# Kernel optimization log

Measured on AMD Instinct MI355X. Metric: run time of the kernel, lower is better.

The kernel has to match this reference:

```python
import jax, jax.numpy as jnp
import numpy as np

B, T, I, H = 32, 1024, 1024, 1024


def _init_cell(key, in_size, hidden):
    k = 1.0 / np.sqrt(hidden)
    k1, k2, k3, k4 = jax.random.split(key, 4)
    Wih = jax.random.uniform(k1, (4 * hidden, in_size), jnp.float32, -k, k)
    Whh = jax.random.uniform(k2, (4 * hidden, hidden), jnp.float32, -k, k)
    bih = jax.random.uniform(k3, (4 * hidden,), jnp.float32, -k, k)
    bhh = jax.random.uniform(k4, (4 * hidden,), jnp.float32, -k, k)
    return Wih, Whh, bih, bhh


def setup_inputs() -> dict:
    key = jax.random.key(0)
    kx, kf, kr = jax.random.split(key, 3)
    x = jax.random.normal(kx, (B, T, I), jnp.float32)
    h0 = jnp.zeros((B, H), jnp.float32)
    c0 = jnp.zeros((B, H), jnp.float32)
    Wih_f, Whh_f, bih_f, bhh_f = _init_cell(kf, I, H)
    Wih_r, Whh_r, bih_r, bhh_r = _init_cell(kr, I, H)
    return {"x": x, "h0": h0, "c0": c0,
            "Wih_f": Wih_f, "Whh_f": Whh_f, "bih_f": bih_f, "bhh_f": bhh_f,
            "Wih_r": Wih_r, "Whh_r": Whh_r, "bih_r": bih_r, "bhh_r": bhh_r}


def _lstm_scan(xs, h0, c0, Wih, Whh, bih, bhh, reverse):
    # xs: [T, B, I]; PyTorch LSTMCell gate order: i, f, g, o
    def step(carry, xt):
        h, c = carry
        gates = xt @ Wih.T + bih + h @ Whh.T + bhh  # [B, 4H]
        i, f, g, o = jnp.split(gates, 4, axis=-1)
        c_new = jax.nn.sigmoid(f) * c + jax.nn.sigmoid(i) * jnp.tanh(g)
        h_new = jax.nn.sigmoid(o) * jnp.tanh(c_new)
        return (h_new, c_new), None

    (hT, cT), _ = jax.lax.scan(step, (h0, c0), xs, reverse=reverse)
    return hT, cT


def reference(x, h0, c0, Wih_f, Whh_f, bih_f, bhh_f, Wih_r, Whh_r, bih_r, bhh_r):
    xs = jnp.swapaxes(x, 0, 1)  # [T, B, I]
    hf, _ = _lstm_scan(xs, h0, c0, Wih_f, Whh_f, bih_f, bhh_f, reverse=False)
    # reversed(x.unbind(1)) == processing time steps from T-1 down to 0
    hr, _ = _lstm_scan(xs, h0, c0, Wih_r, Whh_r, bih_r, bhh_r, reverse=True)
    return (hf, hr)
```

## Files before the change

### kernel.cpp

```cpp
#include <hip/hip_runtime.h>
#include <hip/hip_bf16.h>
#include <cstdint>
#include <cstddef>

typedef unsigned short u16;
typedef unsigned long long u64;
typedef __attribute__((ext_vector_type(8))) short short8;
typedef __attribute__((ext_vector_type(4))) float f32x4;
typedef __attribute__((ext_vector_type(4))) unsigned u32x4;

#define NB 32
#define NT 1024
#define NH 1024
#define TCH 128
#define NCH 8

#define O_XB   0ull
#define O_WIH  67108864ull
#define O_WHHP 83886080ull
#define O_BIAS 117440512ull
#define O_HBUF 117473280ull
#define O_CST  117735424ull
#define O_FLG  117997568ull
#define O_GX   118030336ull
#define DSTRIDE_CH   16777216ull
#define DSTRIDE_HALF 33554432ull
#define DSTRIDE_FULL 134217728ull
#define WS_NEED_HALF (O_GX + 2ull * DSTRIDE_HALF * 2ull)
#define WS_NEED_FULL (O_GX + 2ull * DSTRIDE_FULL * 2ull)

__device__ __forceinline__ u16 f2bf(float f){
  union { float f; unsigned u; } v; v.f = f;
  unsigned r = v.u + 0x7FFFu + ((v.u >> 16) & 1u);
  return (u16)(r >> 16);
}
__device__ __forceinline__ float bf2f(u16 h){
  union { unsigned u; float f; } v; v.u = ((unsigned)h) << 16;
  return v.f;
}
__device__ __forceinline__ float sig_f(float x){ return 1.0f / (1.0f + __expf(-x)); }
__device__ __forceinline__ float tanh_f(float x){ return 1.0f - 2.0f / (1.0f + __expf(2.0f * x)); }

__device__ __forceinline__ void g2l16(const void* g, void* l){
  __builtin_amdgcn_global_load_lds(
      (const __attribute__((address_space(1))) unsigned int*)g,
      (__attribute__((address_space(3))) unsigned int*)l, 16, 0, 0);
}
__device__ __forceinline__ void g2l16c(const void* g, void* l){
  __builtin_amdgcn_global_load_lds(
      (const __attribute__((address_space(1))) unsigned int*)g,
      (__attribute__((address_space(3))) unsigned int*)l, 16, 0, 17);
}
__device__ __forceinline__ void store16_llc(void* p, u32x4 v){
  asm volatile("global_store_dwordx4 %0, %1, off sc0 sc1"
               :: "v"((unsigned long long)(uintptr_t)p), "v"(v) : "memory");
}

__device__ __forceinline__ float sel4(float s0, float s1, float s2, float s3, int k){
  float a = (k & 1) ? s1 : s0;
  float b = (k & 1) ? s3 : s2;
  return (k & 2) ? b : a;
}

__device__ __forceinline__ int img_off(int lr, int bo){
  return lr * 2048 + (bo ^ ((((lr & 7) ^ ((bo >> 8) & 7))) << 4));
}

__global__ void k_cvt(const float* __restrict__ src, u16* __restrict__ dst, int n){
  int i = (blockIdx.x * blockDim.x + threadIdx.x) * 4;
  int stride = gridDim.x * blockDim.x * 4;
  for (; i < n; i += stride){
    float4 v = *(const float4*)(src + i);
    uint2 p;
    p.x = (unsigned)f2bf(v.x) | ((unsigned)f2bf(v.y) << 16);
    p.y = (unsigned)f2bf(v.z) | ((unsigned)f2bf(v.w) << 16);
    *(uint2*)(dst + i) = p;
  }
}

__global__ void k_pack_whh(const float* __restrict__ whh_f, const float* __restrict__ whh_r,
                           u16* __restrict__ dst){
  int bx = blockIdx.x;
  int dir = bx >> 8, rem = bx & 255;
  int jg = rem >> 1, ni = rem & 1;
  const float* whh = dir ? whh_r : whh_f;
  int tid = threadIdx.x;
  int lane = tid & 63, wq = tid >> 6;
  int c = lane & 15;
  int n = (c >> 2) * 1024 + jg * 8 + ni * 4 + (c & 3);
  int kkb = (lane >> 4) * 8;
  size_t fb = ((((size_t)dir * 128 + jg) * 2 + ni) * 32) * 2;
  for (int q = 0; q < 8; q++){
    int ks = wq * 8 + q;
    const float4* p = (const float4*)(whh + (size_t)n * 1024 + ks * 32 + kkb);
    float4 w0 = p[0], w1 = p[1];
    float w[8] = {w0.x, w0.y, w0.z, w0.w, w1.x, w1.y, w1.z, w1.w};
    unsigned hh[4], ll[4];
    #pragma unroll
    for (int e = 0; e < 4; e++){
      u16 h0 = f2bf(w[2*e]),   l0 = f2bf(w[2*e]   - bf2f(f2bf(w[2*e])));
      u16 h1 = f2bf(w[2*e+1]), l1 = f2bf(w[2*e+1] - bf2f(f2bf(w[2*e+1])));
      hh[e] = (unsigned)h0 | ((unsigned)h1 << 16);
      ll[e] = (unsigned)l0 | ((unsigned)l1 << 16);
    }
    uint4* dh = (uint4*)(dst + (fb + (size_t)ks * 2 + 0) * 512 + lane * 8);
    uint4* dl = (uint4*)(dst + (fb + (size_t)ks * 2 + 1) * 512 + lane * 8);
    *dh = make_uint4(hh[0], hh[1], hh[2], hh[3]);
    *dl = make_uint4(ll[0], ll[1], ll[2], ll[3]);
  }
}

__global__ void k_init(const float* __restrict__ h0, const float* __restrict__ c0,
                       const float* __restrict__ bih_f, const float* __restrict__ bhh_f,
                       const float* __restrict__ bih_r, const float* __restrict__ bhh_r,
                       char* __restrict__ hbuf, float* __restrict__ cst,
                       float* __restrict__ bias, int* __restrict__ flg){
  int i = blockIdx.x * blockDim.x + threadIdx.x;
  int stride = gridDim.x * blockDim.x;
  for (int k = i; k < 32768; k += stride){
    int b = k >> 10, j = k & 1023;
    int lr = b & 15, mhb = b >> 4;
    u16 v = f2bf(h0[k]);
    int off = img_off(lr, 2 * j);
    *(u16*)(hbuf + (size_t)((0 * 2 + mhb) * 2) * 32768 + off) = v;
    *(u16*)(hbuf + (size_t)((1 * 2 + mhb) * 2) * 32768 + off) = v;
    float cv = c0[k];
    cst[k] = cv;
    cst[32768 + k] = cv;
  }
  for (int k = i; k < 8192; k += stride){
    if (k < 4096) bias[k] = bih_f[k] + bhh_f[k];
    else          bias[k] = bih_r[k - 4096] + bhh_r[k - 4096];
  }
  for (int k = i; k < 8192; k += stride) flg[k] = 0;
}

__global__ __launch_bounds__(256, 2) void k_gemm(const u16* __restrict__ xb,
                                                 const u16* __restrict__ wih,
                                                 const float* __restrict__ bias,
                                                 u16* __restrict__ gx, int chunk,
                                                 int tOff, size_t dirStride){
  __shared__ u16 smem[2 * 16384];
  const int tid = threadIdx.x;
  const int lane = tid & 63, wid = tid >> 6;
  const int mi = wid >> 1, ni = wid & 1;
  const int c = lane & 15, rg = lane >> 4;
  const int n0 = blockIdx.x * 128;
  const int m0 = blockIdx.y * 128;
  const int dir = blockIdx.z;
  const u16* wd = wih + (size_t)dir * 4194304;

  f32x4 acc[4][4] = {};

  auto stage = [&](int buf, int k0){
    #pragma unroll
    for (int q = 0; q < 8; q++){
      int f = wid * 8 + q;
      int ks = f & 1;
      int kk = k0 + ks * 32 + rg * 8;
      const u16* src;
      if (f < 16){
        int rowloc = (f >> 1) * 16 + c;
        int tl = (m0 + rowloc) >> 5;
        int bb = rowloc & 31;
        int tg = dir ? (1023 - chunk * TCH - tl) : (chunk * TCH + tl);
        src = xb + (size_t)(bb * 1024 + tg) * 1024 + kk;
      } else {
        int nt = (f - 16) >> 1;
        src = wd + (size_t)(n0 + nt * 16 + c) * 1024 + kk;
      }
      g2l16((const void*)src, (void*)(smem + buf * 16384 + f * 512));
    }
  };

  stage(0, 0);
  asm volatile("s_waitcnt vmcnt(0)" ::: "memory");
  __syncthreads();

  for (int it = 0; it < 16; it++){
    int cur = it & 1;
    if (it < 15) stage(cur ^ 1, (it + 1) * 64);
    const u16* bp = smem + cur * 16384;
    #pragma unroll
    for (int ks = 0; ks < 2; ks++){
      short8 a[4], b[4];
      #pragma unroll
      for (int im = 0; im < 4; im++)
        a[im] = *(const short8*)(bp + ((mi * 4 + im) * 2 + ks) * 512 + lane * 8);
      #pragma unroll
      for (int in_ = 0; in_ < 4; in_++)
        b[in_] = *(const short8*)(bp + 8192 + ((ni * 4 + in_) * 2 + ks) * 512 + lane * 8);
      #pragma unroll
      for (int im = 0; im < 4; im++)
        #pragma unroll
        for (int in_ = 0; in_ < 4; in_++)
          acc[im][in_] = __builtin_amdgcn_mfma_f32_16x16x32_bf16(a[im], b[in_], acc[im][in_], 0, 0, 0);
    }
    asm volatile("s_waitcnt vmcnt(0)" ::: "memory");
    __syncthreads();
  }

  u16* T = (u16*)smem;
  const float* bd = bias + dir * 4096;
  #pragma unroll
  for (int in_ = 0; in_ < 4; in_++){
    int nnLocal = (ni * 4 + in_) * 16 + c;
    float bv = bd[n0 + nnLocal];
    #pragma unroll
    for (int im = 0; im < 4; im++){
      #pragma unroll
      for (int r = 0; r < 4; r++){
        int row = (mi * 4 + im) * 16 + rg * 4 + r;
        T[row * 128 + nnLocal] = f2bf(acc[im][in_][r] + bv);
      }
    }
  }
  __syncthreads();
  u16* gxd = gx + (size_t)dir * dirStride;
  const int nprBase = ((n0 & 1023) >> 3) * 32 + ((n0 >> 10) << 3);
  #pragma unroll
  for (int q = 0; q < 8; q++){
    int flat = q * 256 + tid;
    int row = flat >> 4, c16 = flat & 15;
    u32x4 v = *(const u32x4*)(T + row * 128 + c16 * 8);
    *(u32x4*)(gxd + (size_t)(tOff * 32 + m0 + row) * 4096 + nprBase + c16 * 32) = v;
  }
}

__global__ __launch_bounds__(256, 1) void k_rnn(const u16* __restrict__ gx,
                                                const u16* __restrict__ whhp,
                                                char* __restrict__ hbuf,
                                                float* __restrict__ cstate,
                                                float* __restrict__ dout,
                                                int* __restrict__ flg,
                                                int s0, int bar0, int nsteps,
                                                size_t dirStride){
  __shared__ char smem[32768];
  __shared__ __align__(16) u16 tb[16][16];
  __shared__ int lflag[2];
  const int tid = threadIdx.x;
  const int lane = tid & 63, wid = tid >> 6;
  const int bx = blockIdx.x;
  const int dir = bx >> 7, mh = (bx >> 6) & 1, ug = bx & 63;
  const int grp = dir * 2 + mh;
  const int c = lane & 15, rg = lane >> 4;
  const int g = c >> 2, jj = c & 3;
  const int u = ug * 16 + wid * 4 + jj;
  const int jg = ug * 2 + (wid >> 1), ni = wid & 1;

  short8 Bhi[32], Blo[32];
  {
    size_t fb = ((((size_t)dir * 128 + jg) * 2 + ni) * 32) * 2;
    #pragma unroll
    for (int ks = 0; ks < 32; ks++){
      Bhi[ks] = *(const short8*)(whhp + (fb + ks * 2 + 0) * 512 + lane * 8);
      Blo[ks] = *(const short8*)(whhp + (fb + ks * 2 + 1) * 512 + lane * 8);
    }
  }

  float cst[4];
  #pragma unroll
  for (int r = 0; r < 4; r++)
    cst[r] = cstate[(size_t)dir * 32768 + (size_t)(mh * 16 + rg * 4 + r) * 1024 + u];

  const int npr = (u >> 3) * 32 + g * 8 + (u & 7);
  int* flags = flg + grp * 2048;

  if (tid == 0){ lflag[0] = 0; lflag[1] = 0; }
  __syncthreads();

  u16 gxu[4];
  {
    const size_t gof = (size_t)dir * dirStride + npr;
    #pragma unroll
    for (int r = 0; r < 4; r++)
      gxu[r] = gx[gof + (size_t)(mh * 16 + rg * 4 + r) * 4096];
  }

  for (int t = 0; t < nsteps; t++){
    const int s = s0 + t;
    const char* img_r = hbuf + (size_t)(grp * 2 + (s & 1)) * 32768;
    char* img_w = hbuf + (size_t)(grp * 2 + ((s + 1) & 1)) * 32768;
    const unsigned tgt = (unsigned)(bar0 + t);

    if (wid == 0){
      if (t > 0){
        int* fp = flags + (lane & 31) * 32;
        while (true){
          int v = __hip_atomic_load(fp, __ATOMIC_RELAXED, __HIP_MEMORY_SCOPE_AGENT);
          if (__all((unsigned)v >= tgt)) break;
        }
        asm volatile("" ::: "memory");
      }
      #pragma unroll
      for (int i = 0; i < 16; i++)
        g2l16c(img_r + i * 2048 + lane * 16, smem + i * 2048 + lane * 16);
      asm volatile("s_waitcnt vmcnt(0)" ::: "memory");
      __hip_atomic_store(&lflag[0], t + 1, __ATOMIC_RELEASE, __HIP_MEMORY_SCOPE_WORKGROUP);
    } else if (wid == 1){
      if (t > 0){
        int* fp = flags + (32 + (lane & 31)) * 32;
        while (true){
          int v = __hip_atomic_load(fp, __ATOMIC_RELAXED, __HIP_MEMORY_SCOPE_AGENT);
          if (__all((unsigned)v >= tgt)) break;
        }
        asm volatile("" ::: "memory");
      }
      #pragma unroll
      for (int i = 0; i < 16; i++)
        g2l16c(img_r + i * 2048 + 1024 + lane * 16, smem + i * 2048 + 1024 + lane * 16);
      asm volatile("s_waitcnt vmcnt(0)" ::: "memory");
      __hip_atomic_store(&lflag[1], t + 1, __ATOMIC_RELEASE, __HIP_MEMORY_SCOPE_WORKGROUP);
    }

    u16 gxn[4];
    if (t < nsteps - 1){
      const size_t gof = (size_t)dir * dirStride + (size_t)(t + 1) * 131072 + npr;
      #pragma unroll
      for (int r = 0; r < 4; r++)
        gxn[r] = gx[gof + (size_t)(mh * 16 + rg * 4 + r) * 4096];
    }

    f32x4 ah = {0.f,0.f,0.f,0.f}, al = {0.f,0.f,0.f,0.f};
    const int abase = c * 2048;
    while (__hip_atomic_load(&lflag[0], __ATOMIC_ACQUIRE, __HIP_MEMORY_SCOPE_WORKGROUP) < t + 1) {}
    __builtin_amdgcn_sched_barrier(0);
    #pragma unroll
    for (int ks = 0; ks < 16; ks++){
      int b = ks * 64 + rg * 16;
      int addr = abase + (b ^ ((((c & 7) ^ ((b >> 8) & 7))) << 4));
      short8 a = *(const short8*)(smem + addr);
      ah = __builtin_amdgcn_mfma_f32_16x16x32_bf16(a, Bhi[ks], ah, 0, 0, 0);
      al = __builtin_amdgcn_mfma_f32_16x16x32_bf16(a, Blo[ks], al, 0, 0, 0);
    }
    while (__hip_atomic_load(&lflag[1], __ATOMIC_ACQUIRE, __HIP_MEMORY_SCOPE_WORKGROUP) < t + 1) {}
    __builtin_amdgcn_sched_barrier(0);
    #pragma unroll
    for (int ks = 16; ks < 32; ks++){
      int b = ks * 64 + rg * 16;
      int addr = abase + (b ^ ((((c & 7) ^ ((b >> 8) & 7))) << 4));
      short8 a = *(const short8*)(smem + addr);
      ah = __builtin_amdgcn_mfma_f32_16x16x32_bf16(a, Bhi[ks], ah, 0, 0, 0);
      al = __builtin_amdgcn_mfma_f32_16x16x32_bf16(a, Blo[ks], al, 0, 0, 0);
    }

    #pragma unroll
    for (int r = 0; r < 4; r++){
      float v = (ah[r] + al[r]) + bf2f(gxu[r]);
      float act = (g == 2) ? tanh_f(v) : sig_f(v);
      float a4  = __int_as_float(__builtin_amdgcn_ds_swizzle(__float_as_int(act), 0x101F));
      float a8  = __int_as_float(__builtin_amdgcn_ds_swizzle(__float_as_int(act), 0x201F));
      float a12 = __int_as_float(__builtin_amdgcn_ds_swizzle(__float_as_int(act), 0x301F));
      float i_s = sel4(act, a4, a8, a12, g);
      float f_s = sel4(act, a4, a8, a12, g ^ 1);
      float g_t = sel4(act, a4, a8, a12, g ^ 2);
      float o_s = sel4(act, a4, a8, a12, g ^ 3);
      float cn = f_s * cst[r] + i_s * g_t;
      cst[r] = cn;
      float hn = o_s * tanh_f(cn);
      if (g == 0){
        int lr = rg * 4 + r;
        tb[lr][wid * 4 + jj] = f2bf(hn);
        if (s == 1023)
          dout[(size_t)dir * 32768 + (size_t)(mh * 16 + lr) * 1024 + u] = hn;
        if (t == nsteps - 1)
          cstate[(size_t)dir * 32768 + (size_t)(mh * 16 + lr) * 1024 + u] = cn;
      }
    }
    __syncthreads();

    if (wid == 3){
      if (lane < 32){
        int lr = lane >> 1, half = lane & 1;
        u32x4 v = *(const u32x4*)&tb[lr][half * 8];
        store16_llc(img_w + img_off(lr, ug * 32 + half * 16), v);
      }
      asm volatile("s_waitcnt vmcnt(0)" ::: "memory");
      if (lane == 0 && t < nsteps - 1)
        __hip_atomic_store(&flags[ug * 32], bar0 + t + 1,
                           __ATOMIC_RELAXED, __HIP_MEMORY_SCOPE_AGENT);
    }

    if (t < nsteps - 1){
      #pragma unroll
      for (int r = 0; r < 4; r++) gxu[r] = gxn[r];
    }
  }
}

extern "C" void kernel_launch(void* const* d_in, const int* in_sizes, int n_in,
                              void* d_out, int out_size, void* d_ws, size_t ws_size,
                              hipStream_t stream){
  const float* x     = (const float*)d_in[0];
  const float* h0    = (const float*)d_in[1];
  const float* c0    = (const float*)d_in[2];
  const float* Wih_f = (const float*)d_in[3];
  const float* Whh_f = (const float*)d_in[4];
  const float* bih_f = (const float*)d_in[5];
  const float* bhh_f = (const float*)d_in[6];
  const float* Wih_r = (const float*)d_in[7];
  const float* Whh_r = (const float*)d_in[8];
  const float* bih_r = (const float*)d_in[9];
  const float* bhh_r = (const float*)d_in[10];
  float* out = (float*)d_out;

  char* ws = (char*)d_ws;
  u16*   xb    = (u16*)(ws + O_XB);
  u16*   wih   = (u16*)(ws + O_WIH);
  u16*   whhp  = (u16*)(ws + O_WHHP);
  float* bias  = (float*)(ws + O_BIAS);
  char*  hbuf  = (char*)(ws + O_HBUF);
  float* cstw  = (float*)(ws + O_CST);
  int*   flg   = (int*)(ws + O_FLG);
  u16*   gx    = (u16*)(ws + O_GX);

  k_cvt<<<2048, 256, 0, stream>>>(x, xb, 32 * 1024 * 1024);
  k_cvt<<<512, 256, 0, stream>>>(Wih_f, wih, 4096 * 1024);
  k_cvt<<<512, 256, 0, stream>>>(Wih_r, wih + 4194304, 4096 * 1024);
  k_pack_whh<<<512, 256, 0, stream>>>(Whh_f, Whh_r, whhp);
  k_init<<<64, 256, 0, stream>>>(h0, c0, bih_f, bhh_f, bih_r, bhh_r, hbuf, cstw, bias, flg);

  if (ws_size >= WS_NEED_FULL){
    for (int g = 0; g < NCH; g++)
      k_gemm<<<dim3(32, 32, 2), 256, 0, stream>>>(xb, wih, bias, gx, g,
                                                  g * TCH, (size_t)DSTRIDE_FULL);
    k_rnn<<<dim3(256), dim3(256), 0, stream>>>(gx, whhp, hbuf, cstw, out, flg,
                                               0, 0, NT, (size_t)DSTRIDE_FULL);
  } else if (ws_size >= WS_NEED_HALF){
    for (int c2 = 0; c2 < 4; c2++){
      k_gemm<<<dim3(32, 32, 2), 256, 0, stream>>>(xb, wih, bias, gx, 2 * c2,
                                                  0, (size_t)DSTRIDE_HALF);
      k_gemm<<<dim3(32, 32, 2), 256, 0, stream>>>(xb, wih, bias, gx, 2 * c2 + 1,
                                                  128, (size_t)DSTRIDE_HALF);
      k_rnn<<<dim3(256), dim3(256), 0, stream>>>(gx, whhp, hbuf, cstw, out, flg,
                                                 c2 * 256, c2 * 255, 256,
                                                 (size_t)DSTRIDE_HALF);
    }
  } else {
    for (int ch = 0; ch < NCH; ch++){
      k_gemm<<<dim3(32, 32, 2), 256, 0, stream>>>(xb, wih, bias, gx, ch,
                                                  0, (size_t)DSTRIDE_CH);
      k_rnn<<<dim3(256), dim3(256), 0, stream>>>(gx, whhp, hbuf, cstw, out, flg,
                                                 ch * TCH, ch * (TCH - 1), TCH,
                                                 (size_t)DSTRIDE_CH);
    }
  }
}
```

Baseline: 5.558 ms.

## Switch LSTM to single fp16 weights and halve recurrent grid to 128 blocks

```diff
diff --git a/kernel.cpp b/kernel.cpp
--- a/kernel.cpp
+++ b/kernel.cpp
@@ -5,7 +5,7 @@
 
 typedef unsigned short u16;
 typedef unsigned long long u64;
-typedef __attribute__((ext_vector_type(8))) short short8;
+typedef __attribute__((ext_vector_type(8))) _Float16 h8;
 typedef __attribute__((ext_vector_type(4))) float f32x4;
 typedef __attribute__((ext_vector_type(4))) unsigned u32x4;
 
@@ -29,14 +29,11 @@
 #define WS_NEED_HALF (O_GX + 2ull * DSTRIDE_HALF * 2ull)
 #define WS_NEED_FULL (O_GX + 2ull * DSTRIDE_FULL * 2ull)
 
-__device__ __forceinline__ u16 f2bf(float f){
-  union { float f; unsigned u; } v; v.f = f;
-  unsigned r = v.u + 0x7FFFu + ((v.u >> 16) & 1u);
-  return (u16)(r >> 16);
-}
-__device__ __forceinline__ float bf2f(u16 h){
-  union { unsigned u; float f; } v; v.u = ((unsigned)h) << 16;
-  return v.f;
+__device__ __forceinline__ u16 f2h(float f){
+  union { _Float16 h; u16 u; } v; v.h = (_Float16)f; return v.u;
+}
+__device__ __forceinline__ float h2f(u16 b){
+  union { u16 u; _Float16 h; } v; v.u = b; return (float)v.h;
 }
 __device__ __forceinline__ float sig_f(float x){ return 1.0f / (1.0f + __expf(-x)); }
 __device__ __forceinline__ float tanh_f(float x){ return 1.0f - 2.0f / (1.0f + __expf(2.0f * x)); }
@@ -72,8 +69,8 @@
   for (; i < n; i += stride){
     float4 v = *(const float4*)(src + i);
     uint2 p;
-    p.x = (unsigned)f2bf(v.x) | ((unsigned)f2bf(v.y) << 16);
-    p.y = (unsigned)f2bf(v.z) | ((unsigned)f2bf(v.w) << 16);
+    p.x = (unsigned)f2h(v.x) | ((unsigned)f2h(v.y) << 16);
+    p.y = (unsigned)f2h(v.z) | ((unsigned)f2h(v.w) << 16);
     *(uint2*)(dst + i) = p;
   }
 }
@@ -89,24 +86,18 @@
   int c = lane & 15;
   int n = (c >> 2) * 1024 + jg * 8 + ni * 4 + (c & 3);
   int kkb = (lane >> 4) * 8;
-  size_t fb = ((((size_t)dir * 128 + jg) * 2 + ni) * 32) * 2;
+  size_t fb = (((size_t)dir * 128 + jg) * 2 + ni) * 32;
   for (int q = 0; q < 8; q++){
     int ks = wq * 8 + q;
     const float4* p = (const float4*)(whh + (size_t)n * 1024 + ks * 32 + kkb);
     float4 w0 = p[0], w1 = p[1];
     float w[8] = {w0.x, w0.y, w0.z, w0.w, w1.x, w1.y, w1.z, w1.w};
-    unsigned hh[4], ll[4];
-    #pragma unroll
-    for (int e = 0; e < 4; e++){
-      u16 h0 = f2bf(w[2*e]),   l0 = f2bf(w[2*e]   - bf2f(f2bf(w[2*e])));
-      u16 h1 = f2bf(w[2*e+1]), l1 = f2bf(w[2*e+1] - bf2f(f2bf(w[2*e+1])));
-      hh[e] = (unsigned)h0 | ((unsigned)h1 << 16);
-      ll[e] = (unsigned)l0 | ((unsigned)l1 << 16);
-    }
-    uint4* dh = (uint4*)(dst + (fb + (size_t)ks * 2 + 0) * 512 + lane * 8);
-    uint4* dl = (uint4*)(dst + (fb + (size_t)ks * 2 + 1) * 512 + lane * 8);
+    unsigned hh[4];
+    #pragma unroll
+    for (int e = 0; e < 4; e++)
+      hh[e] = (unsigned)f2h(w[2*e]) | ((unsigned)f2h(w[2*e+1]) << 16);
+    uint4* dh = (uint4*)(dst + (fb + (size_t)ks) * 512 + lane * 8);
     *dh = make_uint4(hh[0], hh[1], hh[2], hh[3]);
-    *dl = make_uint4(ll[0], ll[1], ll[2], ll[3]);
   }
 }
 
@@ -120,7 +111,7 @@
   for (int k = i; k < 32768; k += stride){
     int b = k >> 10, j = k & 1023;
     int lr = b & 15, mhb = b >> 4;
-    u16 v = f2bf(h0[k]);
+    u16 v = f2h(h0[k]);
     int off = img_off(lr, 2 * j);
     *(u16*)(hbuf + (size_t)((0 * 2 + mhb) * 2) * 32768 + off) = v;
     *(u16*)(hbuf + (size_t)((1 * 2 + mhb) * 2) * 32768 + off) = v;
@@ -132,7 +123,7 @@
     if (k < 4096) bias[k] = bih_f[k] + bhh_f[k];
     else          bias[k] = bih_r[k - 4096] + bhh_r[k - 4096];
   }
-  for (int k = i; k < 8192; k += stride) flg[k] = 0;
+  for (int k = i; k < 4096; k += stride) flg[k] = 0;
 }
 
 __global__ __launch_bounds__(256, 2) void k_gemm(const u16* __restrict__ xb,
@@ -183,18 +174,18 @@
     const u16* bp = smem + cur * 16384;
     #pragma unroll
     for (int ks = 0; ks < 2; ks++){
-      short8 a[4], b[4];
+      h8 a[4], b[4];
       #pragma unroll
       for (int im = 0; im < 4; im++)
-        a[im] = *(const short8*)(bp + ((mi * 4 + im) * 2 + ks) * 512 + lane * 8);
+        a[im] = *(const h8*)(bp + ((mi * 4 + im) * 2 + ks) * 512 + lane * 8);
       #pragma unroll
       for (int in_ = 0; in_ < 4; in_++)
-        b[in_] = *(const short8*)(bp + 8192 + ((ni * 4 + in_) * 2 + ks) * 512 + lane * 8);
+        b[in_] = *(const h8*)(bp + 8192 + ((ni * 4 + in_) * 2 + ks) * 512 + lane * 8);
       #pragma unroll
       for (int im = 0; im < 4; im++)
         #pragma unroll
         for (int in_ = 0; in_ < 4; in_++)
-          acc[im][in_] = __builtin_amdgcn_mfma_f32_16x16x32_bf16(a[im], b[in_], acc[im][in_], 0, 0, 0);
+          acc[im][in_] = __builtin_amdgcn_mfma_f32_16x16x32_f16(a[im], b[in_], acc[im][in_], 0, 0, 0);
     }
     asm volatile("s_waitcnt vmcnt(0)" ::: "memory");
     __syncthreads();
@@ -211,7 +202,7 @@
       #pragma unroll
       for (int r = 0; r < 4; r++){
         int row = (mi * 4 + im) * 16 + rg * 4 + r;
-        T[row * 128 + nnLocal] = f2bf(acc[im][in_][r] + bv);
+        T[row * 128 + nnLocal] = f2h(acc[im][in_][r] + bv);
       }
     }
   }
@@ -236,45 +227,50 @@
                                                 int s0, int bar0, int nsteps,
                                                 size_t dirStride){
   __shared__ char smem[32768];
-  __shared__ __align__(16) u16 tb[16][16];
+  __shared__ __align__(16) u16 tb[16][32];
   __shared__ int lflag[2];
   const int tid = threadIdx.x;
   const int lane = tid & 63, wid = tid >> 6;
   const int bx = blockIdx.x;
-  const int dir = bx >> 7, mh = (bx >> 6) & 1, ug = bx & 63;
+  const int dir = bx >> 6, mh = (bx >> 5) & 1, ug = bx & 31;
   const int grp = dir * 2 + mh;
   const int c = lane & 15, rg = lane >> 4;
   const int g = c >> 2, jj = c & 3;
-  const int u = ug * 16 + wid * 4 + jj;
-  const int jg = ug * 2 + (wid >> 1), ni = wid & 1;
-
-  short8 Bhi[32], Blo[32];
+  const int jg2 = ug * 4 + wid;
+
+  h8 Bh[32][2];
   {
-    size_t fb = ((((size_t)dir * 128 + jg) * 2 + ni) * 32) * 2;
+    size_t fb0 = (((size_t)dir * 128 + jg2) * 2 + 0) * 32;
+    size_t fb1 = (((size_t)dir * 128 + jg2) * 2 + 1) * 32;
     #pragma unroll
     for (int ks = 0; ks < 32; ks++){
-      Bhi[ks] = *(const short8*)(whhp + (fb + ks * 2 + 0) * 512 + lane * 8);
-      Blo[ks] = *(const short8*)(whhp + (fb + ks * 2 + 1) * 512 + lane * 8);
-    }
-  }
-
-  float cst[4];
+      Bh[ks][0] = *(const h8*)(whhp + (fb0 + ks) * 512 + lane * 8);
+      Bh[ks][1] = *(const h8*)(whhp + (fb1 + ks) * 512 + lane * 8);
+    }
+  }
+
+  float cst[2][4];
   #pragma unroll
-  for (int r = 0; r < 4; r++)
-    cst[r] = cstate[(size_t)dir * 32768 + (size_t)(mh * 16 + rg * 4 + r) * 1024 + u];
-
-  const int npr = (u >> 3) * 32 + g * 8 + (u & 7);
-  int* flags = flg + grp * 2048;
+  for (int it = 0; it < 2; it++)
+    #pragma unroll
+    for (int r = 0; r < 4; r++)
+      cst[it][r] = cstate[(size_t)dir * 32768 +
+                          (size_t)(mh * 16 + rg * 4 + r) * 1024 + jg2 * 8 + it * 4 + jj];
+
+  const int npr0 = jg2 * 32 + g * 8 + jj;
+  int* flags = flg + grp * 1024;
 
   if (tid == 0){ lflag[0] = 0; lflag[1] = 0; }
   __syncthreads();
 
-  u16 gxu[4];
+  u16 gxu[2][4];
   {
-    const size_t gof = (size_t)dir * dirStride + npr;
-    #pragma unroll
-    for (int r = 0; r < 4; r++)
-      gxu[r] = gx[gof + (size_t)(mh * 16 + rg * 4 + r) * 4096];
+    const size_t gof = (size_t)dir * dirStride + npr0;
+    #pragma unroll
+    for (int it = 0; it < 2; it++)
+      #pragma unroll
+      for (int r = 0; r < 4; r++)
+        gxu[it][r] = gx[gof + it * 4 + (size_t)(mh * 16 + rg * 4 + r) * 4096];
   }
 
   for (int t = 0; t < nsteps; t++){
@@ -285,7 +281,7 @@
 
     if (wid == 0){
       if (t > 0){
-        int* fp = flags + (lane & 31) * 32;
+        int* fp = flags + (lane & 15) * 32;
         while (true){
           int v = __hip_atomic_load(fp, __ATOMIC_RELAXED, __HIP_MEMORY_SCOPE_AGENT);
           if (__all((unsigned)v >= tgt)) break;
@@ -299,7 +295,7 @@
       __hip_atomic_store(&lflag[0], t + 1, __ATOMIC_RELEASE, __HIP_MEMORY_SCOPE_WORKGROUP);
     } else if (wid == 1){
       if (t > 0){
-        int* fp = flags + (32 + (lane & 31)) * 32;
+        int* fp = flags + (16 + (lane & 15)) * 32;
         while (true){
           int v = __hip_atomic_load(fp, __ATOMIC_RELAXED, __HIP_MEMORY_SCOPE_AGENT);
           if (__all((unsigned)v >= tgt)) break;
@@ -313,15 +309,17 @@
       __hip_atomic_store(&lflag[1], t + 1, __ATOMIC_RELEASE, __HIP_MEMORY_SCOPE_WORKGROUP);
     }
 
-    u16 gxn[4];
+    u16 gxn[2][4];
     if (t < nsteps - 1){
-      const size_t gof = (size_t)dir * dirStride + (size_t)(t + 1) * 131072 + npr;
-      #pragma unroll
-      for (int r = 0; r < 4; r++)
-        gxn[r] = gx[gof + (size_t)(mh * 16 + rg * 4 + r) * 4096];
-    }
-
-    f32x4 ah = {0.f,0.f,0.f,0.f}, al = {0.f,0.f,0.f,0.f};
+      const size_t gof = (size_t)dir * dirStride + (size_t)(t + 1) * 131072 + npr0;
+      #pragma unroll
+      for (int it = 0; it < 2; it++)
+        #pragma unroll
+        for (int r = 0; r < 4; r++)
+          gxn[it][r] = gx[gof + it * 4 + (size_t)(mh * 16 + rg * 4 + r) * 4096];
+    }
+
+    f32x4 a0 = {0.f,0.f,0.f,0.f}, a1 = {0.f,0.f,0.f,0.f};
     const int abase = c * 2048;
     while (__hip_atomic_load(&lflag[0], __ATOMIC_ACQUIRE, __HIP_MEMORY_SCOPE_WORKGROUP) < t + 1) {}
     __builtin_amdgcn_sched_barrier(0);
@@ -329,9 +327,9 @@
     for (int ks = 0; ks < 16; ks++){
       int b = ks * 64 + rg * 16;
       int addr = abase + (b ^ ((((c & 7) ^ ((b >> 8) & 7))) << 4));
-      short8 a = *(const short8*)(smem + addr);
-      ah = __builtin_amdgcn_mfma_f32_16x16x32_bf16(a, Bhi[ks], ah, 0, 0, 0);
-      al = __builtin_amdgcn_mfma_f32_16x16x32_bf16(a, Blo[ks], al, 0, 0, 0);
+      h8 a = *(const h8*)(smem + addr);
+      a0 = __builtin_amdgcn_mfma_f32_16x16x32_f16(a, Bh[ks][0], a0, 0, 0, 0);
+      a1 = __builtin_amdgcn_mfma_f32_16x16x32_f16(a, Bh[ks][1], a1, 0, 0, 0);
     }
     while (__hip_atomic_load(&lflag[1], __ATOMIC_ACQUIRE, __HIP_MEMORY_SCOPE_WORKGROUP) < t + 1) {}
     __builtin_amdgcn_sched_barrier(0);
@@ -339,42 +337,44 @@
     for (int ks = 16; ks < 32; ks++){
       int b = ks * 64 + rg * 16;
       int addr = abase + (b ^ ((((c & 7) ^ ((b >> 8) & 7))) << 4));
-      short8 a = *(const short8*)(smem + addr);
-      ah = __builtin_amdgcn_mfma_f32_16x16x32_bf16(a, Bhi[ks], ah, 0, 0, 0);
-      al = __builtin_amdgcn_mfma_f32_16x16x32_bf16(a, Blo[ks], al, 0, 0, 0);
-    }
-
-    #pragma unroll
-    for (int r = 0; r < 4; r++){
-      float v = (ah[r] + al[r]) + bf2f(gxu[r]);
-      float act = (g == 2) ? tanh_f(v) : sig_f(v);
-      float a4  = __int_as_float(__builtin_amdgcn_ds_swizzle(__float_as_int(act), 0x101F));
-      float a8  = __int_as_float(__builtin_amdgcn_ds_swizzle(__float_as_int(act), 0x201F));
-      float a12 = __int_as_float(__builtin_amdgcn_ds_swizzle(__float_as_int(act), 0x301F));
-      float i_s = sel4(act, a4, a8, a12, g);
-      float f_s = sel4(act, a4, a8, a12, g ^ 1);
-      float g_t = sel4(act, a4, a8, a12, g ^ 2);
-      float o_s = sel4(act, a4, a8, a12, g ^ 3);
-      float cn = f_s * cst[r] + i_s * g_t;
-      cst[r] = cn;
-      float hn = o_s * tanh_f(cn);
-      if (g == 0){
-        int lr = rg * 4 + r;
-        tb[lr][wid * 4 + jj] = f2bf(hn);
-        if (s == 1023)
-          dout[(size_t)dir * 32768 + (size_t)(mh * 16 + lr) * 1024 + u] = hn;
-        if (t == nsteps - 1)
-          cstate[(size_t)dir * 32768 + (size_t)(mh * 16 + lr) * 1024 + u] = cn;
+      h8 a = *(const h8*)(smem + addr);
+      a0 = __builtin_amdgcn_mfma_f32_16x16x32_f16(a, Bh[ks][0], a0, 0, 0, 0);
+      a1 = __builtin_amdgcn_mfma_f32_16x16x32_f16(a, Bh[ks][1], a1, 0, 0, 0);
+    }
+
+    #pragma unroll
+    for (int it = 0; it < 2; it++){
+      #pragma unroll
+      for (int r = 0; r < 4; r++){
+        float v = (it ? a1[r] : a0[r]) + h2f(gxu[it][r]);
+        float act = (g == 2) ? tanh_f(v) : sig_f(v);
+        float a4  = __int_as_float(__builtin_amdgcn_ds_swizzle(__float_as_int(act), 0x101F));
+        float a8  = __int_as_float(__builtin_amdgcn_ds_swizzle(__float_as_int(act), 0x201F));
+        float a12 = __int_as_float(__builtin_amdgcn_ds_swizzle(__float_as_int(act), 0x301F));
+        float i_s = sel4(act, a4, a8, a12, g);
+        float f_s = sel4(act, a4, a8, a12, g ^ 1);
+        float g_t = sel4(act, a4, a8, a12, g ^ 2);
+        float o_s = sel4(act, a4, a8, a12, g ^ 3);
+        float cn = f_s * cst[it][r] + i_s * g_t;
+        cst[it][r] = cn;
+        float hn = o_s * tanh_f(cn);
+        if (g == 0){
+          int lr = rg * 4 + r;
+          int ub = wid * 8 + it * 4 + jj;
+          tb[lr][ub] = f2h(hn);
+          if (s == 1023)
+            dout[(size_t)dir * 32768 + (size_t)(mh * 16 + lr) * 1024 + ug * 32 + ub] = hn;
+          if (t == nsteps - 1)
+            cstate[(size_t)dir * 32768 + (size_t)(mh * 16 + lr) * 1024 + ug * 32 + ub] = cn;
+        }
       }
     }
     __syncthreads();
 
     if (wid == 3){
-      if (lane < 32){
-        int lr = lane >> 1, half = lane & 1;
-        u32x4 v = *(const u32x4*)&tb[lr][half * 8];
-        store16_llc(img_w + img_off(lr, ug * 32 + half * 16), v);
-      }
+      int lr = lane >> 2, q4 = lane & 3;
+      u32x4 v = *(const u32x4*)&tb[lr][q4 * 8];
+      store16_llc(img_w + img_off(lr, ug * 64 + q4 * 16), v);
       asm volatile("s_waitcnt vmcnt(0)" ::: "memory");
       if (lane == 0 && t < nsteps - 1)
         __hip_atomic_store(&flags[ug * 32], bar0 + t + 1,
@@ -383,7 +383,9 @@
 
     if (t < nsteps - 1){
       #pragma unroll
-      for (int r = 0; r < 4; r++) gxu[r] = gxn[r];
+      for (int it = 0; it < 2; it++)
+        #pragma unroll
+        for (int r = 0; r < 4; r++) gxu[it][r] = gxn[it][r];
     }
   }
 }
@@ -424,7 +426,7 @@
     for (int g = 0; g < NCH; g++)
       k_gemm<<<dim3(32, 32, 2), 256, 0, stream>>>(xb, wih, bias, gx, g,
                                                   g * TCH, (size_t)DSTRIDE_FULL);
-    k_rnn<<<dim3(256), dim3(256), 0, stream>>>(gx, whhp, hbuf, cstw, out, flg,
+    k_rnn<<<dim3(128), dim3(256), 0, stream>>>(gx, whhp, hbuf, cstw, out, flg,
                                                0, 0, NT, (size_t)DSTRIDE_FULL);
   } else if (ws_size >= WS_NEED_HALF){
     for (int c2 = 0; c2 < 4; c2++){
@@ -432,7 +434,7 @@
                                                   0, (size_t)DSTRIDE_HALF);
       k_gemm<<<dim3(32, 32, 2), 256, 0, stream>>>(xb, wih, bias, gx, 2 * c2 + 1,
                                                   128, (size_t)DSTRIDE_HALF);
-      k_rnn<<<dim3(256), dim3(256), 0, stream>>>(gx, whhp, hbuf, cstw, out, flg,
+      k_rnn<<<dim3(128), dim3(256), 0, stream>>>(gx, whhp, hbuf, cstw, out, flg,
                                                  c2 * 256, c2 * 255, 256,
                                                  (size_t)DSTRIDE_HALF);
     }
@@ -440,7 +442,7 @@
     for (int ch = 0; ch < NCH; ch++){
       k_gemm<<<dim3(32, 32, 2), 256, 0, stream>>>(xb, wih, bias, gx, ch,
                                                   0, (size_t)DSTRIDE_CH);
-      k_rnn<<<dim3(256), dim3(256), 0, stream>>>(gx, whhp, hbuf, cstw, out, flg,
+      k_rnn<<<dim3(128), dim3(256), 0, stream>>>(gx, whhp, hbuf, cstw, out, flg,
                                                  ch * TCH, ch * (TCH - 1), TCH,
                                                  (size_t)DSTRIDE_CH);
     }
```

Result: slower. 6.428 ms (+15.7%).

## Switch LSTM matmuls to fp16 and drop split hi/lo recurrent weights

Applied to the files above, without the earlier changes.

```diff
diff --git a/kernel.cpp b/kernel.cpp
--- a/kernel.cpp
+++ b/kernel.cpp
@@ -5,7 +5,7 @@
 
 typedef unsigned short u16;
 typedef unsigned long long u64;
-typedef __attribute__((ext_vector_type(8))) short short8;
+typedef __attribute__((ext_vector_type(8))) _Float16 h8;
 typedef __attribute__((ext_vector_type(4))) float f32x4;
 typedef __attribute__((ext_vector_type(4))) unsigned u32x4;
 
@@ -29,14 +29,11 @@
 #define WS_NEED_HALF (O_GX + 2ull * DSTRIDE_HALF * 2ull)
 #define WS_NEED_FULL (O_GX + 2ull * DSTRIDE_FULL * 2ull)
 
-__device__ __forceinline__ u16 f2bf(float f){
-  union { float f; unsigned u; } v; v.f = f;
-  unsigned r = v.u + 0x7FFFu + ((v.u >> 16) & 1u);
-  return (u16)(r >> 16);
-}
-__device__ __forceinline__ float bf2f(u16 h){
-  union { unsigned u; float f; } v; v.u = ((unsigned)h) << 16;
-  return v.f;
+__device__ __forceinline__ u16 f2h(float f){
+  union { _Float16 h; u16 u; } v; v.h = (_Float16)f; return v.u;
+}
+__device__ __forceinline__ float h2f(u16 b){
+  union { u16 u; _Float16 h; } v; v.u = b; return (float)v.h;
 }
 __device__ __forceinline__ float sig_f(float x){ return 1.0f / (1.0f + __expf(-x)); }
 __device__ __forceinline__ float tanh_f(float x){ return 1.0f - 2.0f / (1.0f + __expf(2.0f * x)); }
@@ -72,8 +69,8 @@
   for (; i < n; i += stride){
     float4 v = *(const float4*)(src + i);
     uint2 p;
-    p.x = (unsigned)f2bf(v.x) | ((unsigned)f2bf(v.y) << 16);
-    p.y = (unsigned)f2bf(v.z) | ((unsigned)f2bf(v.w) << 16);
+    p.x = (unsigned)f2h(v.x) | ((unsigned)f2h(v.y) << 16);
+    p.y = (unsigned)f2h(v.z) | ((unsigned)f2h(v.w) << 16);
     *(uint2*)(dst + i) = p;
   }
 }
@@ -89,24 +86,18 @@
   int c = lane & 15;
   int n = (c >> 2) * 1024 + jg * 8 + ni * 4 + (c & 3);
   int kkb = (lane >> 4) * 8;
-  size_t fb = ((((size_t)dir * 128 + jg) * 2 + ni) * 32) * 2;
+  size_t fb = (((size_t)dir * 128 + jg) * 2 + ni) * 32;
   for (int q = 0; q < 8; q++){
     int ks = wq * 8 + q;
     const float4* p = (const float4*)(whh + (size_t)n * 1024 + ks * 32 + kkb);
     float4 w0 = p[0], w1 = p[1];
     float w[8] = {w0.x, w0.y, w0.z, w0.w, w1.x, w1.y, w1.z, w1.w};
-    unsigned hh[4], ll[4];
-    #pragma unroll
-    for (int e = 0; e < 4; e++){
-      u16 h0 = f2bf(w[2*e]),   l0 = f2bf(w[2*e]   - bf2f(f2bf(w[2*e])));
-      u16 h1 = f2bf(w[2*e+1]), l1 = f2bf(w[2*e+1] - bf2f(f2bf(w[2*e+1])));
-      hh[e] = (unsigned)h0 | ((unsigned)h1 << 16);
-      ll[e] = (unsigned)l0 | ((unsigned)l1 << 16);
-    }
-    uint4* dh = (uint4*)(dst + (fb + (size_t)ks * 2 + 0) * 512 + lane * 8);
-    uint4* dl = (uint4*)(dst + (fb + (size_t)ks * 2 + 1) * 512 + lane * 8);
+    unsigned hh[4];
+    #pragma unroll
+    for (int e = 0; e < 4; e++)
+      hh[e] = (unsigned)f2h(w[2*e]) | ((unsigned)f2h(w[2*e+1]) << 16);
+    uint4* dh = (uint4*)(dst + (fb + (size_t)ks) * 512 + lane * 8);
     *dh = make_uint4(hh[0], hh[1], hh[2], hh[3]);
-    *dl = make_uint4(ll[0], ll[1], ll[2], ll[3]);
   }
 }
 
@@ -120,7 +111,7 @@
   for (int k = i; k < 32768; k += stride){
     int b = k >> 10, j = k & 1023;
     int lr = b & 15, mhb = b >> 4;
-    u16 v = f2bf(h0[k]);
+    u16 v = f2h(h0[k]);
     int off = img_off(lr, 2 * j);
     *(u16*)(hbuf + (size_t)((0 * 2 + mhb) * 2) * 32768 + off) = v;
     *(u16*)(hbuf + (size_t)((1 * 2 + mhb) * 2) * 32768 + off) = v;
@@ -183,18 +174,18 @@
     const u16* bp = smem + cur * 16384;
     #pragma unroll
     for (int ks = 0; ks < 2; ks++){
-      short8 a[4], b[4];
+      h8 a[4], b[4];
       #pragma unroll
       for (int im = 0; im < 4; im++)
-        a[im] = *(const short8*)(bp + ((mi * 4 + im) * 2 + ks) * 512 + lane * 8);
+        a[im] = *(const h8*)(bp + ((mi * 4 + im) * 2 + ks) * 512 + lane * 8);
       #pragma unroll
       for (int in_ = 0; in_ < 4; in_++)
-        b[in_] = *(const short8*)(bp + 8192 + ((ni * 4 + in_) * 2 + ks) * 512 + lane * 8);
+        b[in_] = *(const h8*)(bp + 8192 + ((ni * 4 + in_) * 2 + ks) * 512 + lane * 8);
       #pragma unroll
       for (int im = 0; im < 4; im++)
         #pragma unroll
         for (int in_ = 0; in_ < 4; in_++)
-          acc[im][in_] = __builtin_amdgcn_mfma_f32_16x16x32_bf16(a[im], b[in_], acc[im][in_], 0, 0, 0);
+          acc[im][in_] = __builtin_amdgcn_mfma_f32_16x16x32_f16(a[im], b[in_], acc[im][in_], 0, 0, 0);
     }
     asm volatile("s_waitcnt vmcnt(0)" ::: "memory");
     __syncthreads();
@@ -211,7 +202,7 @@
       #pragma unroll
       for (int r = 0; r < 4; r++){
         int row = (mi * 4 + im) * 16 + rg * 4 + r;
-        T[row * 128 + nnLocal] = f2bf(acc[im][in_][r] + bv);
+        T[row * 128 + nnLocal] = f2h(acc[im][in_][r] + bv);
       }
     }
   }
@@ -248,14 +239,12 @@
   const int u = ug * 16 + wid * 4 + jj;
   const int jg = ug * 2 + (wid >> 1), ni = wid & 1;
 
-  short8 Bhi[32], Blo[32];
+  h8 Bh[32];
   {
-    size_t fb = ((((size_t)dir * 128 + jg) * 2 + ni) * 32) * 2;
-    #pragma unroll
-    for (int ks = 0; ks < 32; ks++){
-      Bhi[ks] = *(const short8*)(whhp + (fb + ks * 2 + 0) * 512 + lane * 8);
-      Blo[ks] = *(const short8*)(whhp + (fb + ks * 2 + 1) * 512 + lane * 8);
-    }
+    size_t fb = (((size_t)dir * 128 + jg) * 2 + ni) * 32;
+    #pragma unroll
+    for (int ks = 0; ks < 32; ks++)
+      Bh[ks] = *(const h8*)(whhp + (fb + ks) * 512 + lane * 8);
   }
 
   float cst[4];
@@ -321,32 +310,38 @@
         gxn[r] = gx[gof + (size_t)(mh * 16 + rg * 4 + r) * 4096];
     }
 
-    f32x4 ah = {0.f,0.f,0.f,0.f}, al = {0.f,0.f,0.f,0.f};
+    f32x4 ae = {0.f,0.f,0.f,0.f}, ao = {0.f,0.f,0.f,0.f};
     const int abase = c * 2048;
     while (__hip_atomic_load(&lflag[0], __ATOMIC_ACQUIRE, __HIP_MEMORY_SCOPE_WORKGROUP) < t + 1) {}
     __builtin_amdgcn_sched_barrier(0);
     #pragma unroll
-    for (int ks = 0; ks < 16; ks++){
-      int b = ks * 64 + rg * 16;
-      int addr = abase + (b ^ ((((c & 7) ^ ((b >> 8) & 7))) << 4));
-      short8 a = *(const short8*)(smem + addr);
-      ah = __builtin_amdgcn_mfma_f32_16x16x32_bf16(a, Bhi[ks], ah, 0, 0, 0);
-      al = __builtin_amdgcn_mfma_f32_16x16x32_bf16(a, Blo[ks], al, 0, 0, 0);
+    for (int kp = 0; kp < 8; kp++){
+      int b0 = (kp * 2) * 64 + rg * 16;
+      int b1 = (kp * 2 + 1) * 64 + rg * 16;
+      int ad0 = abase + (b0 ^ ((((c & 7) ^ ((b0 >> 8) & 7))) << 4));
+      int ad1 = abase + (b1 ^ ((((c & 7) ^ ((b1 >> 8) & 7))) << 4));
+      h8 x0 = *(const h8*)(smem + ad0);
+      h8 x1 = *(const h8*)(smem + ad1);
+      ae = __builtin_amdgcn_mfma_f32_16x16x32_f16(x0, Bh[kp * 2], ae, 0, 0, 0);
+      ao = __builtin_amdgcn_mfma_f32_16x16x32_f16(x1, Bh[kp * 2 + 1], ao, 0, 0, 0);
     }
     while (__hip_atomic_load(&lflag[1], __ATOMIC_ACQUIRE, __HIP_MEMORY_SCOPE_WORKGROUP) < t + 1) {}
     __builtin_amdgcn_sched_barrier(0);
     #pragma unroll
-    for (int ks = 16; ks < 32; ks++){
-      int b = ks * 64 + rg * 16;
-      int addr = abase + (b ^ ((((c & 7) ^ ((b >> 8) & 7))) << 4));
-      short8 a = *(const short8*)(smem + addr);
-      ah = __builtin_amdgcn_mfma_f32_16x16x32_bf16(a, Bhi[ks], ah, 0, 0, 0);
-      al = __builtin_amdgcn_mfma_f32_16x16x32_bf16(a, Blo[ks], al, 0, 0, 0);
+    for (int kp = 8; kp < 16; kp++){
+      int b0 = (kp * 2) * 64 + rg * 16;
+      int b1 = (kp * 2 + 1) * 64 + rg * 16;
+      int ad0 = abase + (b0 ^ ((((c & 7) ^ ((b0 >> 8) & 7))) << 4));
+      int ad1 = abase + (b1 ^ ((((c & 7) ^ ((b1 >> 8) & 7))) << 4));
+      h8 x0 = *(const h8*)(smem + ad0);
+      h8 x1 = *(const h8*)(smem + ad1);
+      ae = __builtin_amdgcn_mfma_f32_16x16x32_f16(x0, Bh[kp * 2], ae, 0, 0, 0);
+      ao = __builtin_amdgcn_mfma_f32_16x16x32_f16(x1, Bh[kp * 2 + 1], ao, 0, 0, 0);
     }
 
     #pragma unroll
     for (int r = 0; r < 4; r++){
-      float v = (ah[r] + al[r]) + bf2f(gxu[r]);
+      float v = (ae[r] + ao[r]) + h2f(gxu[r]);
       float act = (g == 2) ? tanh_f(v) : sig_f(v);
       float a4  = __int_as_float(__builtin_amdgcn_ds_swizzle(__float_as_int(act), 0x101F));
       float a8  = __int_as_float(__builtin_amdgcn_ds_swizzle(__float_as_int(act), 0x201F));
@@ -360,7 +355,7 @@
       float hn = o_s * tanh_f(cn);
       if (g == 0){
         int lr = rg * 4 + r;
-        tb[lr][wid * 4 + jj] = f2bf(hn);
+        tb[lr][wid * 4 + jj] = f2h(hn);
         if (s == 1023)
           dout[(size_t)dir * 32768 + (size_t)(mh * 16 + lr) * 1024 + u] = hn;
         if (t == nsteps - 1)
```

Measured after the change: 4.981 ms. -10.4%, faster.
